# Performance work log

Hardware: AMD Instinct MI355X
Metric: run time of the kernel (lower is better)

Reference implementation:

```python
import jax, jax.numpy as jnp
import numpy as np

NT = 128
T = 262144


def setup_inputs() -> dict:
    key = jax.random.key(0)
    k1, k2, k3, k4, k5 = jax.random.split(key, 5)
    emit = jax.random.normal(k1, (T, NT), dtype=jnp.float32)
    y = jax.random.randint(k2, (T,), 0, NT, dtype=jnp.int64)
    trans = jax.random.normal(k3, (NT, NT), dtype=jnp.float32)
    strans = jax.random.normal(k4, (NT,), dtype=jnp.float32)
    etrans = jax.random.normal(k5, (NT,), dtype=jnp.float32)
    return {"emit": emit, "y": y, "trans": trans, "strans": strans, "etrans": etrans}


def _crf_nll(emit, y, trans, strans, etrans):
    Tlen = emit.shape[0]

    # forward algorithm (log partition) via scan over timesteps 1..T-1
    alpha0 = strans + emit[0]  # [nt]

    def step(alpha, e_t):
        # alpha_new[n] = logsumexp_p(alpha[p] + trans[p, n]) + emit_t[n]
        alpha_new = jax.nn.logsumexp(alpha[:, None] + trans, axis=0) + e_t
        return alpha_new, None

    alpha, _ = jax.lax.scan(step, alpha0, emit[1:])
    logZ = jax.nn.logsumexp(alpha + etrans)

    # gold score (faithful to original: emissions indexed by the *previous* tag)
    prev = y[:-1]
    nxt = y[1:]
    score = strans[y[0]]
    score = score + jnp.sum(trans[prev, nxt] + emit[jnp.arange(Tlen - 1), prev])
    score = score + etrans[y[-1]] + emit[-1, y[-1]]

    return logZ - score


def reference(emit, y, trans, strans, etrans):
    return _crf_nll(emit, y, trans, strans, etrans)
```

## Files before the change

### kernel.cpp

```cpp
#include <hip/hip_runtime.h>

typedef float f32x4 __attribute__((ext_vector_type(4)));

#define T_LEN   262144
#define NTAG    128
#define LCH     8
#define BURN    8
#define NSTEP   16
#define NCHUNK  (T_LEN / LCH)
#define NWAVE   (NCHUNK / 16)
#define NFWDB   (NWAVE / 4)
#define NSCOREB 256
#define C9      6.23832462503951f
#define K63LN2  43.66827237527655f
#define K72LN2  49.90659700060892f

__global__ void crf_setup(const float* __restrict__ trans, uint4* __restrict__ q4)
{
  const int l = threadIdx.x;
  const int col = l & 15, grp = l >> 4;
  for (int rt = 0; rt < 8; ++rt) {
    const int outtag = 16 * rt + col;
    for (int kp = 0; kp < 2; ++kp) {
      unsigned r[4];
      for (int h = 0; h < 2; ++h) {
        const int kt = kp * 2 + h;
        float q[8];
        for (int j = 0; j < 8; ++j) {
          const int k = 32 * kt + 4 * grp + (j & 3) + 16 * (j >> 2);
          q[j] = __expf(trans[k * NTAG + outtag]);
        }
        unsigned lo = (unsigned)__builtin_amdgcn_cvt_pk_fp8_f32(q[0], q[1], 0, false);
        lo = (unsigned)__builtin_amdgcn_cvt_pk_fp8_f32(q[2], q[3], (int)lo, true);
        unsigned hi = (unsigned)__builtin_amdgcn_cvt_pk_fp8_f32(q[4], q[5], 0, false);
        hi = (unsigned)__builtin_amdgcn_cvt_pk_fp8_f32(q[6], q[7], (int)hi, true);
        r[h * 2] = lo; r[h * 2 + 1] = hi;
      }
      q4[(rt * 2 + kp) * 64 + l] = make_uint4(r[0], r[1], r[2], r[3]);
    }
  }
}

__global__ __launch_bounds__(256, 2) void crf_fwd(
    const float* __restrict__ emit, const float* __restrict__ strans,
    const float* __restrict__ etrans, const uint4* __restrict__ q4,
    double* __restrict__ ws)
{
  const int w_id = threadIdx.x >> 6;
  const int l    = threadIdx.x & 63;
  const int col  = l & 15;
  const int grp  = l >> 4;
  const int gw   = blockIdx.x * 4 + w_id;
  const int gc   = gw * 16 + col;

  long a[8][4];
#pragma unroll
  for (int rt = 0; rt < 8; ++rt)
#pragma unroll
    for (int kp = 0; kp < 2; ++kp) {
      uint4 v = q4[(rt * 2 + kp) * 64 + l];
      a[rt][2 * kp]     = (long)(((unsigned long long)v.y << 32) | v.x);
      a[rt][2 * kp + 1] = (long)(((unsigned long long)v.w << 32) | v.z);
    }

  float m0 = 0.f;
  long b[4];
  {
    float u[8][4];
    if (gw == 0) {
      float vm = -1e30f;
#pragma unroll
      for (int rt = 0; rt < 8; ++rt)
#pragma unroll
        for (int r = 0; r < 4; ++r) {
          const int tag = 16 * rt + 4 * grp + r;
          u[rt][r] = (col == 0) ? (strans[tag] + emit[tag]) : 0.f;
          vm = fmaxf(vm, u[rt][r]);
        }
      vm = fmaxf(vm, __shfl_xor(vm, 16, 64));
      vm = fmaxf(vm, __shfl_xor(vm, 32, 64));
      m0 = vm;
#pragma unroll
      for (int rt = 0; rt < 8; ++rt)
#pragma unroll
        for (int r = 0; r < 4; ++r)
          u[rt][r] = (col == 0) ? __expf(u[rt][r] - vm) : 1.0f;
    } else {
#pragma unroll
      for (int rt = 0; rt < 8; ++rt)
#pragma unroll
        for (int r = 0; r < 4; ++r) u[rt][r] = 1.0f;
    }
#pragma unroll
    for (int kt = 0; kt < 4; ++kt) {
      unsigned lo = (unsigned)__builtin_amdgcn_cvt_pk_fp8_f32(u[2*kt][0], u[2*kt][1], 0, false);
      lo = (unsigned)__builtin_amdgcn_cvt_pk_fp8_f32(u[2*kt][2], u[2*kt][3], (int)lo, true);
      unsigned hi = (unsigned)__builtin_amdgcn_cvt_pk_fp8_f32(u[2*kt+1][0], u[2*kt+1][1], 0, false);
      hi = (unsigned)__builtin_amdgcn_cvt_pk_fp8_f32(u[2*kt+1][2], u[2*kt+1][3], (int)hi, true);
      b[kt] = (long)(((unsigned long long)hi << 32) | lo);
    }
  }

  const int t0 = (gc == 0) ? 1 : (gc * LCH - BURN);
  float4 pf[2][8];
  {
    const float* e0 = emit + ((size_t)t0 << 7) + 4 * grp;
    const float* e1 = emit + ((size_t)(t0 + 1) << 7) + 4 * grp;
#pragma unroll
    for (int rt = 0; rt < 8; ++rt) {
      pf[0][rt] = *(const float4*)(e0 + 16 * rt);
      pf[1][rt] = *(const float4*)(e1 + 16 * rt);
    }
  }

  float acc = 0.f;

#pragma unroll
  for (int s = 0; s < NSTEP; ++s) {
    float e[8][4];
#pragma unroll
    for (int rt = 0; rt < 8; ++rt) {
      e[rt][0] = __expf(pf[s & 1][rt].x - C9);
      e[rt][1] = __expf(pf[s & 1][rt].y - C9);
      e[rt][2] = __expf(pf[s & 1][rt].z - C9);
      e[rt][3] = __expf(pf[s & 1][rt].w - C9);
    }
    if (s < NSTEP - 2) {
      const float* ep = emit + ((size_t)(t0 + s + 2) << 7) + 4 * grp;
#pragma unroll
      for (int rt = 0; rt < 8; ++rt) pf[s & 1][rt] = *(const float4*)(ep + 16 * rt);
    }

    f32x4 c[8];
#pragma unroll
    for (int rt = 0; rt < 8; ++rt) c[rt] = (f32x4){0.f, 0.f, 0.f, 0.f};
#pragma unroll
    for (int kt = 0; kt < 4; ++kt)
#pragma unroll
      for (int rt = 0; rt < 8; ++rt)
        c[rt] = __builtin_amdgcn_mfma_f32_16x16x32_fp8_fp8(a[rt][kt], b[kt], c[rt], 0, 0, 0);

    float w[8][4];
#pragma unroll
    for (int rt = 0; rt < 8; ++rt)
#pragma unroll
      for (int r = 0; r < 4; ++r) w[rt][r] = c[rt][r] * e[rt][r];

    if ((s & 3) == 3) {
      float vm = w[0][0];
#pragma unroll
      for (int rt = 0; rt < 8; ++rt)
#pragma unroll
        for (int r = 0; r < 4; ++r) vm = fmaxf(vm, w[rt][r]);
      vm = fmaxf(vm, __shfl_xor(vm, 16, 64));
      vm = fmaxf(vm, __shfl_xor(vm, 32, 64));
      const float lv = __logf(vm);
      if (s == 3)  acc += (gc == 0) ? lv : 0.f;
      if (s == 11) acc += (gc != 0) ? lv : 0.f;
      if (s == 15) acc += (gc != 0) ? lv : 0.f;
      const float rinv = __builtin_amdgcn_rcpf(vm);
#pragma unroll
      for (int rt = 0; rt < 8; ++rt)
#pragma unroll
        for (int r = 0; r < 4; ++r) w[rt][r] *= rinv;

      if (s == NSTEP - 1 && gw == NWAVE - 1) {
        float lse = 0.f;
#pragma unroll
        for (int rt = 0; rt < 8; ++rt)
#pragma unroll
          for (int r = 0; r < 4; ++r)
            lse += w[rt][r] * __expf(etrans[16 * rt + 4 * grp + r]);
        lse += __shfl_xor(lse, 16, 64);
        lse += __shfl_xor(lse, 32, 64);
        if (l == 15) atomicAdd(&ws[2], (double)lse);
      }
    }
    if (s == 6) {
      if (gw == 0) {
        float vm = w[0][0];
#pragma unroll
        for (int rt = 0; rt < 8; ++rt)
#pragma unroll
          for (int r = 0; r < 4; ++r) vm = fmaxf(vm, w[rt][r]);
        vm = fmaxf(vm, __shfl_xor(vm, 16, 64));
        vm = fmaxf(vm, __shfl_xor(vm, 32, 64));
        acc += (gc == 0) ? __logf(vm) : 0.f;
      }
    }

#pragma unroll
    for (int kt = 0; kt < 4; ++kt) {
      unsigned lo = (unsigned)__builtin_amdgcn_cvt_pk_fp8_f32(w[2*kt][0], w[2*kt][1], 0, false);
      lo = (unsigned)__builtin_amdgcn_cvt_pk_fp8_f32(w[2*kt][2], w[2*kt][3], (int)lo, true);
      unsigned hi = (unsigned)__builtin_amdgcn_cvt_pk_fp8_f32(w[2*kt+1][0], w[2*kt+1][1], 0, false);
      hi = (unsigned)__builtin_amdgcn_cvt_pk_fp8_f32(w[2*kt+1][2], w[2*kt+1][3], (int)hi, true);
      b[kt] = (long)(((unsigned long long)hi << 32) | lo);
    }
  }

  const float accf = acc + ((gc == 0) ? (m0 + K63LN2) : K72LN2);
  float av = (grp == 0) ? accf : 0.f;
#pragma unroll
  for (int off = 1; off < 64; off <<= 1) av += __shfl_xor(av, off, 64);
  if (l == 0) atomicAdd(&ws[0], (double)av);
}

__global__ void crf_score(const float* __restrict__ emit, const int* __restrict__ y,
                          const float* __restrict__ trans, const float* __restrict__ strans,
                          const float* __restrict__ etrans, double* __restrict__ ws)
{
  __shared__ float sred[4];
  int idx0 = blockIdx.x * 256 + threadIdx.x;
  float v = 0.f;
  for (int t = idx0; t < T_LEN - 1; t += NSCOREB * 256) {
    int yt = y[t], yn = y[t + 1];
    v += trans[yt * NTAG + yn] + emit[(size_t)t * NTAG + yt];
  }
  if (idx0 == 0) {
    int yl = y[T_LEN - 1];
    v += strans[y[0]] + etrans[yl] + emit[(size_t)(T_LEN - 1) * NTAG + yl];
  }
#pragma unroll
  for (int off = 1; off < 64; off <<= 1) v += __shfl_xor(v, off, 64);
  if ((threadIdx.x & 63) == 0) sred[threadIdx.x >> 6] = v;
  __syncthreads();
  if (threadIdx.x == 0)
    atomicAdd(&ws[1], (double)(sred[0] + sred[1] + sred[2] + sred[3]));
}

__global__ void crf_final(const double* __restrict__ ws, float* __restrict__ out)
{
  out[0] = (float)(ws[0] + log(ws[2]) - ws[1]);
}

extern "C" void kernel_launch(void* const* d_in, const int* in_sizes, int n_in,
                              void* d_out, int out_size, void* d_ws, size_t ws_size,
                              hipStream_t stream)
{
  const float* emit   = (const float*)d_in[0];
  const int*   y      = (const int*)d_in[1];
  const float* trans  = (const float*)d_in[2];
  const float* strans = (const float*)d_in[3];
  const float* etrans = (const float*)d_in[4];
  float*  out = (float*)d_out;
  double* ws  = (double*)d_ws;
  uint4*  q4  = (uint4*)((char*)d_ws + 64);

  hipMemsetAsync(ws, 0, 4 * sizeof(double), stream);
  crf_setup<<<dim3(1), dim3(64), 0, stream>>>(trans, q4);
  crf_score<<<dim3(NSCOREB), dim3(256), 0, stream>>>(emit, y, trans, strans, etrans, ws);
  crf_fwd<<<dim3(NFWDB), dim3(256), 0, stream>>>(emit, strans, etrans, q4, ws);
  crf_final<<<dim3(1), dim3(1), 0, stream>>>(ws, out);
}
```

Before: 82.38 us.

## Fuse score, forward and final kernels; stage fp8 emissions through LDS

Merges the gold-score, forward-algorithm and finalisation kernels into one launch, using a last-block atomic counter to write the output. Each block cooperatively loads its 520 emission rows with coalesced float4 reads, exponentiates them and packs them to fp8 in swizzled LDS. The forward steps then read emissions from LDS instead of issuing strided per-lane global loads. Scaling constants are split between the transition matrix and the emissions to keep values in fp8 range. This removes two launches and the scattered global traffic, at the cost of extra fp8 precision loss on emissions, about 66 KB of LDS per block, and a serial load phase before compute.

```diff
diff --git a/kernel.cpp b/kernel.cpp
--- a/kernel.cpp
+++ b/kernel.cpp
@@ -1,6 +1,7 @@
 #include <hip/hip_runtime.h>
 
 typedef float f32x4 __attribute__((ext_vector_type(4)));
+typedef float f32x2 __attribute__((ext_vector_type(2)));
 
 #define T_LEN   262144
 #define NTAG    128
@@ -8,10 +9,10 @@
 #define BURN    8
 #define NSTEP   16
 #define NCHUNK  (T_LEN / LCH)
-#define NWAVE   (NCHUNK / 16)
-#define NFWDB   (NWAVE / 4)
-#define NSCOREB 256
-#define C9      6.23832462503951f
+#define NFWDB   512
+#define ROWS_PB 520
+#define C5      3.465735902799726f
+#define C4      2.772588722239781f
 #define K63LN2  43.66827237527655f
 #define K72LN2  49.90659700060892f
 
@@ -28,7 +29,7 @@
         float q[8];
         for (int j = 0; j < 8; ++j) {
           const int k = 32 * kt + 4 * grp + (j & 3) + 16 * (j >> 2);
-          q[j] = __expf(trans[k * NTAG + outtag]);
+          q[j] = __expf(trans[k * NTAG + outtag] - C4);
         }
         unsigned lo = (unsigned)__builtin_amdgcn_cvt_pk_fp8_f32(q[0], q[1], 0, false);
         lo = (unsigned)__builtin_amdgcn_cvt_pk_fp8_f32(q[2], q[3], (int)lo, true);
@@ -41,17 +42,44 @@
   }
 }
 
-__global__ __launch_bounds__(256, 2) void crf_fwd(
-    const float* __restrict__ emit, const float* __restrict__ strans,
+__global__ __launch_bounds__(256, 2) void crf_main(
+    const float* __restrict__ emit, const int* __restrict__ y,
+    const float* __restrict__ trans, const float* __restrict__ strans,
     const float* __restrict__ etrans, const uint4* __restrict__ q4,
-    double* __restrict__ ws)
+    double* __restrict__ ws, float* __restrict__ out)
 {
-  const int w_id = threadIdx.x >> 6;
-  const int l    = threadIdx.x & 63;
-  const int col  = l & 15;
-  const int grp  = l >> 4;
-  const int gw   = blockIdx.x * 4 + w_id;
-  const int gc   = gw * 16 + col;
+  __shared__ unsigned int elds[ROWS_PB * 32];
+
+  const int tid = threadIdx.x;
+  const int blk = blockIdx.x;
+
+  {
+    const long rowbase = (long)blk * 512 - 8;
+    const float4* em4 = (const float4*)emit;
+#pragma unroll 4
+    for (int i = 0; i < 65; ++i) {
+      const int f  = tid + 256 * i;
+      const int lr = f >> 5;
+      const int q  = f & 31;
+      long grow = rowbase + lr; if (grow < 0) grow = 0;
+      const float4 v = em4[grow * 32 + q];
+      const float e0 = __expf(v.x - C5), e1 = __expf(v.y - C5);
+      const float e2 = __expf(v.z - C5), e3 = __expf(v.w - C5);
+      unsigned d = (unsigned)__builtin_amdgcn_cvt_pk_fp8_f32(e0, e1, 0, false);
+      d = (unsigned)__builtin_amdgcn_cvt_pk_fp8_f32(e2, e3, (int)d, true);
+      const int g = q & 3, rt = q >> 2;
+      const int slot = (2 * g + (rt >> 2)) ^ ((lr >> 3) & 7);
+      elds[lr * 32 + slot * 4 + (rt & 3)] = d;
+    }
+  }
+  __syncthreads();
+
+  const int w   = tid >> 6;
+  const int l   = tid & 63;
+  const int col = l & 15;
+  const int g   = l >> 4;
+  const int gw  = blk * 4 + w;
+  const int gc  = gw * 16 + col;
 
   long a[8][4];
 #pragma unroll
@@ -64,7 +92,7 @@
     }
 
   float m0 = 0.f;
-  long b[4];
+  long bb[4];
   {
     float u[8][4];
     if (gw == 0) {
@@ -73,7 +101,7 @@
       for (int rt = 0; rt < 8; ++rt)
 #pragma unroll
         for (int r = 0; r < 4; ++r) {
-          const int tag = 16 * rt + 4 * grp + r;
+          const int tag = 16 * rt + 4 * g + r;
           u[rt][r] = (col == 0) ? (strans[tag] + emit[tag]) : 0.f;
           vm = fmaxf(vm, u[rt][r]);
         }
@@ -97,61 +125,50 @@
       lo = (unsigned)__builtin_amdgcn_cvt_pk_fp8_f32(u[2*kt][2], u[2*kt][3], (int)lo, true);
       unsigned hi = (unsigned)__builtin_amdgcn_cvt_pk_fp8_f32(u[2*kt+1][0], u[2*kt+1][1], 0, false);
       hi = (unsigned)__builtin_amdgcn_cvt_pk_fp8_f32(u[2*kt+1][2], u[2*kt+1][3], (int)hi, true);
-      b[kt] = (long)(((unsigned long long)hi << 32) | lo);
-    }
-  }
-
-  const int t0 = (gc == 0) ? 1 : (gc * LCH - BURN);
-  float4 pf[2][8];
-  {
-    const float* e0 = emit + ((size_t)t0 << 7) + 4 * grp;
-    const float* e1 = emit + ((size_t)(t0 + 1) << 7) + 4 * grp;
+      bb[kt] = (long)(((unsigned long long)hi << 32) | lo);
+    }
+  }
+
+  int lrb = (16 * w + col) * 8;
+  if (gc == 0) lrb = 9;
+
+  float acc = 0.f;
+
+#pragma unroll
+  for (int s = 0; s < NSTEP; ++s) {
+    const int lr = lrb + s;
+    const int sw = (lr >> 3) & 7;
+    const uint4 E0 = *(const uint4*)&elds[lr * 32 + (((2 * g + 0) ^ sw) << 2)];
+    const uint4 E1 = *(const uint4*)&elds[lr * 32 + (((2 * g + 1) ^ sw) << 2)];
+
+    f32x4 c[8];
+#pragma unroll
+    for (int rt = 0; rt < 8; ++rt) c[rt] = (f32x4){0.f, 0.f, 0.f, 0.f};
+#pragma unroll
+    for (int kt = 0; kt < 4; ++kt)
+#pragma unroll
+      for (int rt = 0; rt < 8; ++rt)
+        c[rt] = __builtin_amdgcn_mfma_f32_16x16x32_fp8_fp8(a[rt][kt], bb[kt], c[rt], 0, 0, 0);
+
+    float wv[8][4];
 #pragma unroll
     for (int rt = 0; rt < 8; ++rt) {
-      pf[0][rt] = *(const float4*)(e0 + 16 * rt);
-      pf[1][rt] = *(const float4*)(e1 + 16 * rt);
-    }
-  }
-
-  float acc = 0.f;
-
-#pragma unroll
-  for (int s = 0; s < NSTEP; ++s) {
-    float e[8][4];
-#pragma unroll
-    for (int rt = 0; rt < 8; ++rt) {
-      e[rt][0] = __expf(pf[s & 1][rt].x - C9);
-      e[rt][1] = __expf(pf[s & 1][rt].y - C9);
-      e[rt][2] = __expf(pf[s & 1][rt].z - C9);
-      e[rt][3] = __expf(pf[s & 1][rt].w - C9);
-    }
-    if (s < NSTEP - 2) {
-      const float* ep = emit + ((size_t)(t0 + s + 2) << 7) + 4 * grp;
-#pragma unroll
-      for (int rt = 0; rt < 8; ++rt) pf[s & 1][rt] = *(const float4*)(ep + 16 * rt);
-    }
-
-    f32x4 c[8];
-#pragma unroll
-    for (int rt = 0; rt < 8; ++rt) c[rt] = (f32x4){0.f, 0.f, 0.f, 0.f};
-#pragma unroll
-    for (int kt = 0; kt < 4; ++kt)
-#pragma unroll
-      for (int rt = 0; rt < 8; ++rt)
-        c[rt] = __builtin_amdgcn_mfma_f32_16x16x32_fp8_fp8(a[rt][kt], b[kt], c[rt], 0, 0, 0);
-
-    float w[8][4];
-#pragma unroll
-    for (int rt = 0; rt < 8; ++rt)
-#pragma unroll
-      for (int r = 0; r < 4; ++r) w[rt][r] = c[rt][r] * e[rt][r];
+      const unsigned dw = (rt < 4) ? ((const unsigned*)&E0)[rt & 3]
+                                   : ((const unsigned*)&E1)[rt & 3];
+      const f32x2 lo = __builtin_amdgcn_cvt_pk_f32_fp8((int)dw, false);
+      const f32x2 hi = __builtin_amdgcn_cvt_pk_f32_fp8((int)dw, true);
+      wv[rt][0] = c[rt][0] * lo[0];
+      wv[rt][1] = c[rt][1] * lo[1];
+      wv[rt][2] = c[rt][2] * hi[0];
+      wv[rt][3] = c[rt][3] * hi[1];
+    }
 
     if ((s & 3) == 3) {
-      float vm = w[0][0];
-#pragma unroll
-      for (int rt = 0; rt < 8; ++rt)
-#pragma unroll
-        for (int r = 0; r < 4; ++r) vm = fmaxf(vm, w[rt][r]);
+      float vm = wv[0][0];
+#pragma unroll
+      for (int rt = 0; rt < 8; ++rt)
+#pragma unroll
+        for (int r = 0; r < 4; ++r) vm = fmaxf(vm, wv[rt][r]);
       vm = fmaxf(vm, __shfl_xor(vm, 16, 64));
       vm = fmaxf(vm, __shfl_xor(vm, 32, 64));
       const float lv = __logf(vm);
@@ -162,76 +179,80 @@
 #pragma unroll
       for (int rt = 0; rt < 8; ++rt)
 #pragma unroll
-        for (int r = 0; r < 4; ++r) w[rt][r] *= rinv;
-
-      if (s == NSTEP - 1 && gw == NWAVE - 1) {
+        for (int r = 0; r < 4; ++r) wv[rt][r] *= rinv;
+
+      if (s == NSTEP - 1 && gw == (NCHUNK / 16) - 1) {
         float lse = 0.f;
 #pragma unroll
         for (int rt = 0; rt < 8; ++rt)
 #pragma unroll
           for (int r = 0; r < 4; ++r)
-            lse += w[rt][r] * __expf(etrans[16 * rt + 4 * grp + r]);
+            lse += wv[rt][r] * __expf(etrans[16 * rt + 4 * g + r]);
         lse += __shfl_xor(lse, 16, 64);
         lse += __shfl_xor(lse, 32, 64);
         if (l == 15) atomicAdd(&ws[2], (double)lse);
       }
     }
-    if (s == 6) {
-      if (gw == 0) {
-        float vm = w[0][0];
-#pragma unroll
-        for (int rt = 0; rt < 8; ++rt)
-#pragma unroll
-          for (int r = 0; r < 4; ++r) vm = fmaxf(vm, w[rt][r]);
-        vm = fmaxf(vm, __shfl_xor(vm, 16, 64));
-        vm = fmaxf(vm, __shfl_xor(vm, 32, 64));
-        acc += (gc == 0) ? __logf(vm) : 0.f;
+    if (s == 6 && gw == 0) {
+      float vm = wv[0][0];
+#pragma unroll
+      for (int rt = 0; rt < 8; ++rt)
+#pragma unroll
+        for (int r = 0; r < 4; ++r) vm = fmaxf(vm, wv[rt][r]);
+      vm = fmaxf(vm, __shfl_xor(vm, 16, 64));
+      vm = fmaxf(vm, __shfl_xor(vm, 32, 64));
+      acc += (gc == 0) ? __logf(vm) : 0.f;
+    }
+
+#pragma unroll
+    for (int kt = 0; kt < 4; ++kt) {
+      unsigned lo = (unsigned)__builtin_amdgcn_cvt_pk_fp8_f32(wv[2*kt][0], wv[2*kt][1], 0, false);
+      lo = (unsigned)__builtin_amdgcn_cvt_pk_fp8_f32(wv[2*kt][2], wv[2*kt][3], (int)lo, true);
+      unsigned hi = (unsigned)__builtin_amdgcn_cvt_pk_fp8_f32(wv[2*kt+1][0], wv[2*kt+1][1], 0, false);
+      hi = (unsigned)__builtin_amdgcn_cvt_pk_fp8_f32(wv[2*kt+1][2], wv[2*kt+1][3], (int)hi, true);
+      bb[kt] = (long)(((unsigned long long)hi << 32) | lo);
+    }
+  }
+
+  {
+    const float accf = acc + ((gc == 0) ? (m0 + K63LN2) : K72LN2);
+    float av = (g == 0) ? accf : 0.f;
+#pragma unroll
+    for (int off = 1; off < 64; off <<= 1) av += __shfl_xor(av, off, 64);
+    if (l == 0) atomicAdd(&ws[0], (double)av);
+  }
+
+  {
+    float sv = 0.f;
+#pragma unroll
+    for (int ii = 0; ii < 2; ++ii) {
+      const int t = blk * 512 + tid + 256 * ii;
+      if (t < T_LEN - 1) {
+        const int yt = y[t], yn = y[t + 1];
+        sv += trans[yt * NTAG + yn] + emit[(size_t)t * NTAG + yt];
       }
     }
-
-#pragma unroll
-    for (int kt = 0; kt < 4; ++kt) {
-      unsigned lo = (unsigned)__builtin_amdgcn_cvt_pk_fp8_f32(w[2*kt][0], w[2*kt][1], 0, false);
-      lo = (unsigned)__builtin_amdgcn_cvt_pk_fp8_f32(w[2*kt][2], w[2*kt][3], (int)lo, true);
-      unsigned hi = (unsigned)__builtin_amdgcn_cvt_pk_fp8_f32(w[2*kt+1][0], w[2*kt+1][1], 0, false);
-      hi = (unsigned)__builtin_amdgcn_cvt_pk_fp8_f32(w[2*kt+1][2], w[2*kt+1][3], (int)hi, true);
-      b[kt] = (long)(((unsigned long long)hi << 32) | lo);
-    }
-  }
-
-  const float accf = acc + ((gc == 0) ? (m0 + K63LN2) : K72LN2);
-  float av = (grp == 0) ? accf : 0.f;
-#pragma unroll
-  for (int off = 1; off < 64; off <<= 1) av += __shfl_xor(av, off, 64);
-  if (l == 0) atomicAdd(&ws[0], (double)av);
-}
-
-__global__ void crf_score(const float* __restrict__ emit, const int* __restrict__ y,
-                          const float* __restrict__ trans, const float* __restrict__ strans,
-                          const float* __restrict__ etrans, double* __restrict__ ws)
-{
-  __shared__ float sred[4];
-  int idx0 = blockIdx.x * 256 + threadIdx.x;
-  float v = 0.f;
-  for (int t = idx0; t < T_LEN - 1; t += NSCOREB * 256) {
-    int yt = y[t], yn = y[t + 1];
-    v += trans[yt * NTAG + yn] + emit[(size_t)t * NTAG + yt];
-  }
-  if (idx0 == 0) {
-    int yl = y[T_LEN - 1];
-    v += strans[y[0]] + etrans[yl] + emit[(size_t)(T_LEN - 1) * NTAG + yl];
-  }
-#pragma unroll
-  for (int off = 1; off < 64; off <<= 1) v += __shfl_xor(v, off, 64);
-  if ((threadIdx.x & 63) == 0) sred[threadIdx.x >> 6] = v;
+    if (blk == 0 && tid == 0) sv += strans[y[0]];
+    if (blk == NFWDB - 1 && tid == 0) {
+      const int yl = y[T_LEN - 1];
+      sv += etrans[yl] + emit[(size_t)(T_LEN - 1) * NTAG + yl];
+    }
+#pragma unroll
+    for (int off = 1; off < 64; off <<= 1) sv += __shfl_xor(sv, off, 64);
+    if (l == 0) atomicAdd(&ws[1], (double)sv);
+  }
+
   __syncthreads();
-  if (threadIdx.x == 0)
-    atomicAdd(&ws[1], (double)(sred[0] + sred[1] + sred[2] + sred[3]));
-}
-
-__global__ void crf_final(const double* __restrict__ ws, float* __restrict__ out)
-{
-  out[0] = (float)(ws[0] + log(ws[2]) - ws[1]);
+  if (tid == 0) {
+    __threadfence();
+    const unsigned t = atomicAdd((unsigned*)&ws[3], 1u);
+    if (t == NFWDB - 1) {
+      const double d0 = atomicAdd(&ws[0], 0.0);
+      const double d1 = atomicAdd(&ws[1], 0.0);
+      const double d2 = atomicAdd(&ws[2], 0.0);
+      out[0] = (float)(d0 + log(d2) - d1);
+    }
+  }
 }
 
 extern "C" void kernel_launch(void* const* d_in, const int* in_sizes, int n_in,
@@ -249,7 +270,6 @@
 
   hipMemsetAsync(ws, 0, 4 * sizeof(double), stream);
   crf_setup<<<dim3(1), dim3(64), 0, stream>>>(trans, q4);
-  crf_score<<<dim3(NSCOREB), dim3(256), 0, stream>>>(emit, y, trans, strans, etrans, ws);
-  crf_fwd<<<dim3(NFWDB), dim3(256), 0, stream>>>(emit, strans, etrans, q4, ws);
-  crf_final<<<dim3(1), dim3(1), 0, stream>>>(ws, out);
+  crf_main<<<dim3(NFWDB), dim3(256), 0, stream>>>(
+      emit, y, trans, strans, etrans, q4, ws, out);
 }
```

New measurement: 98.52 us. +19.6%, slower.

## Fuse gold-score and finalize into forward kernel with last-block completion

Applied to the files above, without the earlier changes.

Merges the score and final kernels into the forward kernel. The last block to finish, found through an atomic counter, writes the output, which removes two launches and the gaps between them. The forward step now renormalizes every step instead of every fourth step. Block indices are swizzled, and launch bounds are raised to 4 blocks per SM. The extra per-step max, shuffles and log add ALU and cross-lane work, and the tighter register cap risks spills given the large MFMA operand arrays.

```diff
diff --git a/kernel.cpp b/kernel.cpp
--- a/kernel.cpp
+++ b/kernel.cpp
@@ -6,19 +6,17 @@
 #define NTAG    128
 #define LCH     8
 #define BURN    8
-#define NSTEP   16
+#define NSTEP   (LCH + BURN)
 #define NCHUNK  (T_LEN / LCH)
 #define NWAVE   (NCHUNK / 16)
 #define NFWDB   (NWAVE / 4)
-#define NSCOREB 256
 #define C9      6.23832462503951f
 #define K63LN2  43.66827237527655f
 #define K72LN2  49.90659700060892f
 
 __global__ void crf_setup(const float* __restrict__ trans, uint4* __restrict__ q4)
 {
-  const int l = threadIdx.x;
-  const int col = l & 15, grp = l >> 4;
+  const int l = threadIdx.x, col = l & 15, grp = l >> 4;
   for (int rt = 0; rt < 8; ++rt) {
     const int outtag = 16 * rt + col;
     for (int kp = 0; kp < 2; ++kp) {
@@ -41,16 +39,18 @@
   }
 }
 
-__global__ __launch_bounds__(256, 2) void crf_fwd(
-    const float* __restrict__ emit, const float* __restrict__ strans,
+__global__ __launch_bounds__(256, 4) void crf_all(
+    const float* __restrict__ emit, const int* __restrict__ y,
+    const float* __restrict__ trans, const float* __restrict__ strans,
     const float* __restrict__ etrans, const uint4* __restrict__ q4,
-    double* __restrict__ ws)
+    double* __restrict__ ws, float* __restrict__ out)
 {
+  const int blk  = ((int)blockIdx.x & 7) * (NFWDB / 8) + ((int)blockIdx.x >> 3);
   const int w_id = threadIdx.x >> 6;
   const int l    = threadIdx.x & 63;
   const int col  = l & 15;
   const int grp  = l >> 4;
-  const int gw   = blockIdx.x * 4 + w_id;
+  const int gw   = blk * 4 + w_id;
   const int gc   = gw * 16 + col;
 
   long a[8][4];
@@ -140,98 +140,85 @@
       for (int rt = 0; rt < 8; ++rt)
         c[rt] = __builtin_amdgcn_mfma_f32_16x16x32_fp8_fp8(a[rt][kt], b[kt], c[rt], 0, 0, 0);
 
-    float w[8][4];
+    float wv[8][4];
+    float vm = -1e30f;
 #pragma unroll
     for (int rt = 0; rt < 8; ++rt)
 #pragma unroll
-      for (int r = 0; r < 4; ++r) w[rt][r] = c[rt][r] * e[rt][r];
-
-    if ((s & 3) == 3) {
-      float vm = w[0][0];
-#pragma unroll
-      for (int rt = 0; rt < 8; ++rt)
-#pragma unroll
-        for (int r = 0; r < 4; ++r) vm = fmaxf(vm, w[rt][r]);
-      vm = fmaxf(vm, __shfl_xor(vm, 16, 64));
-      vm = fmaxf(vm, __shfl_xor(vm, 32, 64));
-      const float lv = __logf(vm);
-      if (s == 3)  acc += (gc == 0) ? lv : 0.f;
-      if (s == 11) acc += (gc != 0) ? lv : 0.f;
-      if (s == 15) acc += (gc != 0) ? lv : 0.f;
-      const float rinv = __builtin_amdgcn_rcpf(vm);
-#pragma unroll
-      for (int rt = 0; rt < 8; ++rt)
-#pragma unroll
-        for (int r = 0; r < 4; ++r) w[rt][r] *= rinv;
-
-      if (s == NSTEP - 1 && gw == NWAVE - 1) {
-        float lse = 0.f;
-#pragma unroll
-        for (int rt = 0; rt < 8; ++rt)
-#pragma unroll
-          for (int r = 0; r < 4; ++r)
-            lse += w[rt][r] * __expf(etrans[16 * rt + 4 * grp + r]);
-        lse += __shfl_xor(lse, 16, 64);
-        lse += __shfl_xor(lse, 32, 64);
-        if (l == 15) atomicAdd(&ws[2], (double)lse);
+      for (int r = 0; r < 4; ++r) {
+        wv[rt][r] = c[rt][r] * e[rt][r];
+        vm = fmaxf(vm, wv[rt][r]);
       }
-    }
-    if (s == 6) {
-      if (gw == 0) {
-        float vm = w[0][0];
-#pragma unroll
-        for (int rt = 0; rt < 8; ++rt)
-#pragma unroll
-          for (int r = 0; r < 4; ++r) vm = fmaxf(vm, w[rt][r]);
-        vm = fmaxf(vm, __shfl_xor(vm, 16, 64));
-        vm = fmaxf(vm, __shfl_xor(vm, 32, 64));
-        acc += (gc == 0) ? __logf(vm) : 0.f;
+    vm = fmaxf(vm, __shfl_xor(vm, 16, 64));
+    vm = fmaxf(vm, __shfl_xor(vm, 32, 64));
+    const bool on = (gc == 0) ? (s <= LCH - 2) : (s >= BURN);
+    if (on) acc += __logf(vm);
+    const float rinv = __frcp_rn(vm);
+#pragma unroll
+    for (int kt = 0; kt < 4; ++kt) {
+      const float s0 = wv[2*kt][0] * rinv,   s1 = wv[2*kt][1] * rinv;
+      const float s2 = wv[2*kt][2] * rinv,   s3 = wv[2*kt][3] * rinv;
+      const float s4 = wv[2*kt+1][0] * rinv, s5 = wv[2*kt+1][1] * rinv;
+      const float s6 = wv[2*kt+1][2] * rinv, s7 = wv[2*kt+1][3] * rinv;
+      unsigned lo = (unsigned)__builtin_amdgcn_cvt_pk_fp8_f32(s0, s1, 0, false);
+      lo = (unsigned)__builtin_amdgcn_cvt_pk_fp8_f32(s2, s3, (int)lo, true);
+      unsigned hi = (unsigned)__builtin_amdgcn_cvt_pk_fp8_f32(s4, s5, 0, false);
+      hi = (unsigned)__builtin_amdgcn_cvt_pk_fp8_f32(s6, s7, (int)hi, true);
+      b[kt] = (long)(((unsigned long long)hi << 32) | lo);
+    }
+
+    if (s == NSTEP - 1 && gw == NWAVE - 1) {
+      float lse = 0.f;
+#pragma unroll
+      for (int rt = 0; rt < 8; ++rt)
+#pragma unroll
+        for (int r = 0; r < 4; ++r)
+          lse += (wv[rt][r] * rinv) * __expf(etrans[16 * rt + 4 * grp + r]);
+      lse += __shfl_xor(lse, 16, 64);
+      lse += __shfl_xor(lse, 32, 64);
+      if (l == 15) atomicAdd(&ws[2], (double)lse);
+    }
+  }
+
+  {
+    const float accf = acc + ((gc == 0) ? (m0 + K63LN2) : K72LN2);
+    float av = (grp == 0) ? accf : 0.f;
+#pragma unroll
+    for (int off = 1; off < 64; off <<= 1) av += __shfl_xor(av, off, 64);
+    if (l == 0) atomicAdd(&ws[0], (double)av);
+  }
+
+  {
+    float sv = 0.f;
+    const int base = (int)blockIdx.x * 512 + threadIdx.x;
+#pragma unroll
+    for (int ii = 0; ii < 2; ++ii) {
+      const int t = base + 256 * ii;
+      if (t < T_LEN - 1) {
+        const int yt = y[t], yn = y[t + 1];
+        sv += trans[yt * NTAG + yn] + emit[(size_t)t * NTAG + yt];
       }
     }
-
-#pragma unroll
-    for (int kt = 0; kt < 4; ++kt) {
-      unsigned lo = (unsigned)__builtin_amdgcn_cvt_pk_fp8_f32(w[2*kt][0], w[2*kt][1], 0, false);
-      lo = (unsigned)__builtin_amdgcn_cvt_pk_fp8_f32(w[2*kt][2], w[2*kt][3], (int)lo, true);
-      unsigned hi = (unsigned)__builtin_amdgcn_cvt_pk_fp8_f32(w[2*kt+1][0], w[2*kt+1][1], 0, false);
-      hi = (unsigned)__builtin_amdgcn_cvt_pk_fp8_f32(w[2*kt+1][2], w[2*kt+1][3], (int)hi, true);
-      b[kt] = (long)(((unsigned long long)hi << 32) | lo);
-    }
-  }
-
-  const float accf = acc + ((gc == 0) ? (m0 + K63LN2) : K72LN2);
-  float av = (grp == 0) ? accf : 0.f;
-#pragma unroll
-  for (int off = 1; off < 64; off <<= 1) av += __shfl_xor(av, off, 64);
-  if (l == 0) atomicAdd(&ws[0], (double)av);
-}
-
-__global__ void crf_score(const float* __restrict__ emit, const int* __restrict__ y,
-                          const float* __restrict__ trans, const float* __restrict__ strans,
-                          const float* __restrict__ etrans, double* __restrict__ ws)
-{
-  __shared__ float sred[4];
-  int idx0 = blockIdx.x * 256 + threadIdx.x;
-  float v = 0.f;
-  for (int t = idx0; t < T_LEN - 1; t += NSCOREB * 256) {
-    int yt = y[t], yn = y[t + 1];
-    v += trans[yt * NTAG + yn] + emit[(size_t)t * NTAG + yt];
-  }
-  if (idx0 == 0) {
-    int yl = y[T_LEN - 1];
-    v += strans[y[0]] + etrans[yl] + emit[(size_t)(T_LEN - 1) * NTAG + yl];
-  }
-#pragma unroll
-  for (int off = 1; off < 64; off <<= 1) v += __shfl_xor(v, off, 64);
-  if ((threadIdx.x & 63) == 0) sred[threadIdx.x >> 6] = v;
+    if (blockIdx.x == 0 && threadIdx.x == 0) {
+      const int yl = y[T_LEN - 1];
+      sv += strans[y[0]] + etrans[yl] + emit[(size_t)(T_LEN - 1) * NTAG + yl];
+    }
+#pragma unroll
+    for (int off = 1; off < 64; off <<= 1) sv += __shfl_xor(sv, off, 64);
+    if (l == 0) atomicAdd(&ws[1], (double)sv);
+  }
+
   __syncthreads();
-  if (threadIdx.x == 0)
-    atomicAdd(&ws[1], (double)(sred[0] + sred[1] + sred[2] + sred[3]));
-}
-
-__global__ void crf_final(const double* __restrict__ ws, float* __restrict__ out)
-{
-  out[0] = (float)(ws[0] + log(ws[2]) - ws[1]);
+  if (threadIdx.x == 0) {
+    __threadfence();
+    const unsigned t = atomicAdd((unsigned*)&ws[3], 1u);
+    if (t == NFWDB - 1) {
+      const double d0 = atomicAdd(&ws[0], 0.0);
+      const double d1 = atomicAdd(&ws[1], 0.0);
+      const double d2 = atomicAdd(&ws[2], 0.0);
+      out[0] = (float)(d0 + log(d2) - d1);
+    }
+  }
 }
 
 extern "C" void kernel_launch(void* const* d_in, const int* in_sizes, int n_in,
@@ -245,11 +232,10 @@
   const float* etrans = (const float*)d_in[4];
   float*  out = (float*)d_out;
   double* ws  = (double*)d_ws;
-  uint4*  q4  = (uint4*)((char*)d_ws + 64);
+  uint4*  q4  = (uint4*)((char*)d_ws + 128);
 
   hipMemsetAsync(ws, 0, 4 * sizeof(double), stream);
   crf_setup<<<dim3(1), dim3(64), 0, stream>>>(trans, q4);
-  crf_score<<<dim3(NSCOREB), dim3(256), 0, stream>>>(emit, y, trans, strans, etrans, ws);
-  crf_fwd<<<dim3(NFWDB), dim3(256), 0, stream>>>(emit, strans, etrans, q4, ws);
-  crf_final<<<dim3(1), dim3(1), 0, stream>>>(ws, out);
+  crf_all<<<dim3(NFWDB), dim3(256), 0, stream>>>(
+      emit, y, trans, strans, etrans, q4, ws, out);
 }
```

Measured after the change: 120.9 us. +46.8%, slower.
